# Optimization experiments

Hardware: AMD Instinct MI355X
Metric: run time of the kernel (lower is better)

## Reference

```python
import jax, jax.numpy as jnp
import numpy as np

B, C, H, W = 4, 256, 64, 64
CH = C // 2  # inner channels


def setup_inputs() -> dict:
    key = jax.random.key(0)
    ks = jax.random.split(key, 9)
    s_in = 1.0 / np.sqrt(C)
    s_w = 1.0 / np.sqrt(CH)
    return {
        "x": jax.random.normal(ks[0], (B, C, H, W), dtype=jnp.float32),
        "theta_w": jax.random.normal(ks[1], (CH, C), dtype=jnp.float32) * s_in,
        "theta_b": jax.random.normal(ks[2], (CH,), dtype=jnp.float32) * s_in,
        "phi_w": jax.random.normal(ks[3], (CH, C), dtype=jnp.float32) * s_in,
        "phi_b": jax.random.normal(ks[4], (CH,), dtype=jnp.float32) * s_in,
        "g_w": jax.random.normal(ks[5], (CH, C), dtype=jnp.float32) * s_in,
        "g_b": jax.random.normal(ks[6], (CH,), dtype=jnp.float32) * s_in,
        "W_w": jax.random.normal(ks[7], (C, CH), dtype=jnp.float32) * s_w,
        "W_b": jax.random.normal(ks[8], (C,), dtype=jnp.float32) * s_w,
    }


def _proj(x_flat, w, b):
    # 1x1 conv == channel matmul; x_flat: [B, C, N] -> [B, O, N]
    return jnp.einsum("oc,bcn->bon", w, x_flat) + b[None, :, None]


def reference(x, theta_w, theta_b, phi_w, phi_b, g_w, g_b, W_w, W_b):
    b, c, h, w = x.shape
    n = h * w
    xf = x.reshape(b, c, n)
    theta = _proj(xf, theta_w, theta_b)  # [B, CH, N]
    phi = _proj(xf, phi_w, phi_b)        # [B, CH, N]
    g = _proj(xf, g_w, g_b)              # [B, CH, N]
    # scores[b,i,j] = theta[:, :, i] . phi[:, :, j]; softmax over j
    attn = jax.nn.softmax(jnp.einsum("bci,bcj->bij", theta, phi), axis=-1)
    # torch: bmm(g_x, attn) -> out[b,c,i] = sum_j g[b,c,j] * attn[b,j,i]
    out = jnp.einsum("bcj,bji->bci", g, attn)  # [B, CH, N]
    out = jnp.einsum("oc,bcn->bon", W_w, out) + W_b[None, :, None]
    return out.reshape(b, c, h, w) + x
```

## Files before the change

### kernel.cpp

```cpp
#include <hip/hip_runtime.h>
#include <hip/hip_bf16.h>
#include <math.h>

#define BB    4
#define CC    256
#define CHN   128
#define NN    4096

typedef short short8 __attribute__((ext_vector_type(8)));
typedef float f32x4  __attribute__((ext_vector_type(4)));
typedef float f32x16 __attribute__((ext_vector_type(16)));
typedef unsigned short u16;
typedef u16  us4 __attribute__((ext_vector_type(4)));

#define MFMA16(a, b, c) __builtin_amdgcn_mfma_f32_16x16x32_bf16((a), (b), (c), 0, 0, 0)
#define MFMA32(a, b, c) __builtin_amdgcn_mfma_f32_32x32x16_bf16((a), (b), (c), 0, 0, 0)
#define LOG2E 1.4426950408889634f

#if __has_builtin(__builtin_amdgcn_exp2f)
#define EXP2F(x) __builtin_amdgcn_exp2f(x)
#else
#define EXP2F(x) exp2f(x)
#endif
#if __has_builtin(__builtin_amdgcn_logf)
#define LOG2F(x) __builtin_amdgcn_logf(x)
#else
#define LOG2F(x) log2f(x)
#endif

static __device__ __forceinline__ u16 f2bf(float f) {
    union { float f; unsigned u; } v; v.f = f;
    unsigned r = v.u + 0x7FFFu + ((v.u >> 16) & 1u);
    return (u16)(r >> 16);
}
static __device__ __forceinline__ unsigned pkbf(float a, float b) {
    __hip_bfloat162 h = __float22bfloat162_rn(make_float2(a, b));
    return *reinterpret_cast<unsigned*>(&h);
}
static __device__ __forceinline__ int sw128(int row, int u) {
    return row * 128 + ((u ^ (row & 7)) << 3);
}
static __device__ __forceinline__ void gload16(const u16* g, u16* l) {
    __builtin_amdgcn_global_load_lds(
        (const __attribute__((address_space(1))) void*)g,
        (__attribute__((address_space(3))) void*)l, 16, 0, 0);
}

typedef union { unsigned u[4]; short8 v; } bfrag;

#if __has_builtin(__builtin_amdgcn_permlane32_swap)
#define REPACK(sv, f) do { \
    unsigned e0 = pkbf(EXP2F(sv[0]),  EXP2F(sv[1])); \
    unsigned e1 = pkbf(EXP2F(sv[2]),  EXP2F(sv[3])); \
    unsigned e2 = pkbf(EXP2F(sv[4]),  EXP2F(sv[5])); \
    unsigned e3 = pkbf(EXP2F(sv[6]),  EXP2F(sv[7])); \
    unsigned e4 = pkbf(EXP2F(sv[8]),  EXP2F(sv[9])); \
    unsigned e5 = pkbf(EXP2F(sv[10]), EXP2F(sv[11])); \
    unsigned e6 = pkbf(EXP2F(sv[12]), EXP2F(sv[13])); \
    unsigned e7 = pkbf(EXP2F(sv[14]), EXP2F(sv[15])); \
    auto r02 = __builtin_amdgcn_permlane32_swap(e0, e2, false, false); \
    auto r13 = __builtin_amdgcn_permlane32_swap(e1, e3, false, false); \
    auto r46 = __builtin_amdgcn_permlane32_swap(e4, e6, false, false); \
    auto r57 = __builtin_amdgcn_permlane32_swap(e5, e7, false, false); \
    f[0].u[0] = r02[0]; f[0].u[1] = r13[0]; \
    f[0].u[2] = r02[1]; f[0].u[3] = r13[1]; \
    f[1].u[0] = r46[0]; f[1].u[1] = r57[0]; \
    f[1].u[2] = r46[1]; f[1].u[3] = r57[1]; \
} while (0)
#else
#define REPACK(sv, f) do { \
    unsigned e0 = pkbf(EXP2F(sv[0]),  EXP2F(sv[1])); \
    unsigned e1 = pkbf(EXP2F(sv[2]),  EXP2F(sv[3])); \
    unsigned e2 = pkbf(EXP2F(sv[4]),  EXP2F(sv[5])); \
    unsigned e3 = pkbf(EXP2F(sv[6]),  EXP2F(sv[7])); \
    unsigned e4 = pkbf(EXP2F(sv[8]),  EXP2F(sv[9])); \
    unsigned e5 = pkbf(EXP2F(sv[10]), EXP2F(sv[11])); \
    unsigned e6 = pkbf(EXP2F(sv[12]), EXP2F(sv[13])); \
    unsigned e7 = pkbf(EXP2F(sv[14]), EXP2F(sv[15])); \
    unsigned q0 = __shfl_xor(e0, 32), q1 = __shfl_xor(e1, 32); \
    unsigned q2 = __shfl_xor(e2, 32), q3 = __shfl_xor(e3, 32); \
    unsigned q4 = __shfl_xor(e4, 32), q5 = __shfl_xor(e5, 32); \
    unsigned q6 = __shfl_xor(e6, 32), q7 = __shfl_xor(e7, 32); \
    f[0].u[0] = lh ? q2 : e0;  f[0].u[1] = lh ? q3 : e1; \
    f[0].u[2] = lh ? e2 : q0;  f[0].u[3] = lh ? e3 : q1; \
    f[1].u[0] = lh ? q6 : e4;  f[1].u[1] = lh ? q7 : e5; \
    f[1].u[2] = lh ? e6 : q4;  f[1].u[3] = lh ? e7 : q5; \
} while (0)
#endif

__global__ __launch_bounds__(256) void k_cvtw(
    const float* __restrict__ tw, const float* __restrict__ pw,
    const float* __restrict__ gw, const float* __restrict__ Ww,
    u16* __restrict__ wall)
{
    int idx = (blockIdx.x * 256 + threadIdx.x) * 4;
    const float* s = (idx < 32768) ? tw
                   : (idx < 65536) ? pw
                   : (idx < 98304) ? gw : Ww;
    float sc = (idx < 32768) ? LOG2E : 1.0f;
    float4 v = *(const float4*)(s + (idx & 32767));
    us4 r = { f2bf(v.x * sc), f2bf(v.y * sc), f2bf(v.z * sc), f2bf(v.w * sc) };
    *(us4*)(wall + idx) = r;
}

__global__ __launch_bounds__(512) void k_proj(
    const float* __restrict__ x, const u16* __restrict__ wall,
    const float* __restrict__ tb, const float* __restrict__ pb,
    const float* __restrict__ gbias,
    u16* __restrict__ tht, u16* __restrict__ pht, u16* __restrict__ gg)
{
    __shared__ u16 xs[64 * 264];
    __shared__ u16 gbuf[128 * 68];
    const int tid = threadIdx.x;
    const int n0  = blockIdx.x * 64;
    const int b   = blockIdx.y;
    const int ln  = tid & 15, q = (tid >> 4) & 3, wid = tid >> 6;
    const int ow  = wid & 1, nw = wid >> 1;

    for (int p = 0; p < 8; ++p) {
        int id = p * 512 + tid;
        int c = id >> 4, n4 = (id & 15) * 4;
        float4 xv = *(const float4*)(x + ((size_t)b * CC + c) * NN + n0 + n4);
        xs[(n4 + 0) * 264 + c] = f2bf(xv.x);
        xs[(n4 + 1) * 264 + c] = f2bf(xv.y);
        xs[(n4 + 2) * 264 + c] = f2bf(xv.z);
        xs[(n4 + 3) * 264 + c] = f2bf(xv.w);
    }
    __syncthreads();

    short8 bfr[8];
    #pragma unroll
    for (int ks = 0; ks < 8; ++ks)
        bfr[ks] = *(const short8*)(&xs[(nw * 16 + ln) * 264 + ks * 32 + q * 8]);

    for (int pr = 0; pr < 3; ++pr) {
        const u16* wsrc = wall + pr * 32768;
        f32x4 acc[4];
        #pragma unroll
        for (int oo = 0; oo < 4; ++oo) acc[oo] = (f32x4){0.f, 0.f, 0.f, 0.f};
        for (int ks = 0; ks < 8; ++ks) {
            short8 a[4];
            #pragma unroll
            for (int oo = 0; oo < 4; ++oo)
                a[oo] = *(const short8*)(wsrc + (size_t)(ow*64 + oo*16 + ln) * 256 + ks*32 + q*8);
            #pragma unroll
            for (int oo = 0; oo < 4; ++oo)
                acc[oo] = MFMA16(a[oo], bfr[ks], acc[oo]);
        }
        const float* bias = (pr == 0) ? tb : (pr == 1 ? pb : gbias);
        const float bsc = (pr == 0) ? LOG2E : 1.0f;
        if (pr < 2) {
            u16* dst = (pr == 0) ? tht : pht;
            const int n = n0 + nw * 16 + ln;
            #pragma unroll
            for (int oo = 0; oo < 4; ++oo) {
                int o = ow * 64 + oo * 16 + q * 4;
                float4 bv = *(const float4*)(bias + o);
                f32x4 v = acc[oo];
                uint2 r = { pkbf(v.x + bv.x * bsc, v.y + bv.y * bsc),
                            pkbf(v.z + bv.z * bsc, v.w + bv.w * bsc) };
                *(uint2*)(dst + ((size_t)b * NN + n) * CHN + o) = r;
            }
        } else {
            const int nl = nw * 16 + ln;
            #pragma unroll
            for (int oo = 0; oo < 4; ++oo) {
                int o = ow * 64 + oo * 16 + q * 4;
                float4 bv = *(const float4*)(bias + o);
                f32x4 v = acc[oo];
                gbuf[(o + 0) * 68 + nl] = f2bf(v.x + bv.x);
                gbuf[(o + 1) * 68 + nl] = f2bf(v.y + bv.y);
                gbuf[(o + 2) * 68 + nl] = f2bf(v.z + bv.z);
                gbuf[(o + 3) * 68 + nl] = f2bf(v.w + bv.w);
            }
            __syncthreads();
            for (int p = 0; p < 4; ++p) {
                int id = p * 512 + tid;
                int c = id >> 4, n4 = (id & 15) * 4;
                us4 r = *(const us4*)(&gbuf[c * 68 + n4]);
                *(us4*)(gg + ((size_t)b * CHN + c) * NN + n0 + n4) = r;
            }
        }
    }
}

__global__ __launch_bounds__(512, 2) void k_rowsum(
    const u16* __restrict__ tht, const u16* __restrict__ pht,
    float* __restrict__ Z)
{
    __shared__ u16 ph_s[2][128 * 128];
    const int tid = threadIdx.x;
    const int j0  = blockIdx.x * 256;
    const int i00 = blockIdx.y * 1024;
    const int b   = blockIdx.z;
    const int l   = tid & 63, w = tid >> 6;
    const int lm  = l & 31, lh = l >> 5;
    const u16* thb = tht + (size_t)b * NN * CHN;
    const u16* phb = pht + (size_t)b * NN * CHN;

    short8 ar[8];
    #pragma unroll
    for (int ks = 0; ks < 8; ++ks)
        ar[ks] = *(const short8*)(thb + (size_t)(j0 + w*32 + lm) * CHN + ks*16 + lh*8);

    for (int p = 0; p < 4; ++p) {
        int id = p * 512 + tid;
        int row = id >> 4, u = id & 15;
        short8 v = *(const short8*)(phb + (size_t)(i00 + row) * CHN + u * 8);
        *(short8*)(&ph_s[0][sw128(row, u)]) = v;
    }

    float zp[16];
    #pragma unroll
    for (int r = 0; r < 16; ++r) zp[r] = 0.f;

    for (int is = 0; is < 8; ++is) {
        __syncthreads();
        if (is < 7) {
            for (int p = 0; p < 4; ++p) {
                int id = p * 512 + tid;
                int row = id >> 4, u = id & 15;
                short8 v = *(const short8*)(phb + (size_t)(i00 + (is+1)*128 + row) * CHN + u * 8);
                *(short8*)(&ph_s[(is + 1) & 1][sw128(row, u)]) = v;
            }
        }
        const u16* cur = ph_s[is & 1];

        #pragma unroll
        for (int ii = 0; ii < 4; ++ii) {
            f32x16 s;
            #pragma unroll
            for (int r = 0; r < 16; ++r) s[r] = 0.f;
            #pragma unroll
            for (int ks = 0; ks < 8; ++ks) {
                short8 bfrag = *(const short8*)(&cur[sw128(ii*32 + lm, ks*2 + lh)]);
                s = MFMA32(ar[ks], bfrag, s);
            }
            #pragma unroll
            for (int r = 0; r < 16; ++r) zp[r] += EXP2F(s[r]);
        }
    }

    float zr[16];
    #pragma unroll
    for (int r = 0; r < 16; ++r) {
        float v = zp[r];
        v += __shfl_xor(v, 1);
        v += __shfl_xor(v, 2);
        v += __shfl_xor(v, 4);
        v += __shfl_xor(v, 8);
        v += __shfl_xor(v, 16);
        zr[r] = v;
    }
    if (lm == 0) {
        #pragma unroll
        for (int r = 0; r < 16; ++r) {
            int j = j0 + w*32 + (r & 3) + 8*(r >> 2) + 4*lh;
            atomicAdd(&Z[(size_t)b * NN + j], zr[r]);
        }
    }
}

__global__ __launch_bounds__(256) void k_log(
    const float* __restrict__ Z, float* __restrict__ L)
{
    int idx = (blockIdx.x * 256 + threadIdx.x) * 4;
    float4 z = *(const float4*)(Z + idx);
    float4 r = { -LOG2F(z.x), -LOG2F(z.y), -LOG2F(z.z), -LOG2F(z.w) };
    *(float4*)(L + idx) = r;
}

__global__ __launch_bounds__(256, 2) void k_attn(
    const u16* __restrict__ tht, const u16* __restrict__ pht,
    const u16* __restrict__ gg, const float* __restrict__ Lbuf,
    u16* __restrict__ innerT)
{
    __shared__ u16 th_s[2][32 * 128];
    __shared__ u16 g_s [2][64 * 64];
    const int tid = threadIdx.x;
    const int i0  = blockIdx.x * 128;
    const int jq  = blockIdx.y;
    const int b   = blockIdx.z;
    const int w   = tid >> 6;
    const int lm  = tid & 31, lh = (tid >> 5) & 1;

    const u16*  thb = tht + (size_t)b * NN * CHN;
    const u16*  ggb = gg  + (size_t)b * CHN * NN;
    const float* Lb = Lbuf + (size_t)b * NN;

    int offT[2], offG[2];
    #pragma unroll
    for (int p = 0; p < 2; ++p) {
        int id = p * 256 + tid;
        int rT = id >> 4, uT = (id & 15) ^ (rT & 7);
        offT[p] = rT * CHN + uT * 8;
        int R = id >> 3, gi = (id & 7) ^ (R & 7);
        offG[p] = (((R << 1) | (gi >> 2)) * NN) + (gi & 3) * 8;
    }

    short8 phr[8];
    #pragma unroll
    for (int ks = 0; ks < 8; ++ks)
        phr[ks] = *(const short8*)(pht + ((size_t)b * NN + i0 + w*32 + lm) * CHN + ks*16 + lh*8);

    #pragma unroll
    for (int p = 0; p < 2; ++p) {
        gload16(thb + (size_t)(jq * 512) * CHN + offT[p], &th_s[0][0] + p*2048 + tid*8);
        gload16(ggb + jq * 512 + offG[p],                 &g_s [0][0] + p*2048 + tid*8);
    }
    __syncthreads();

    f32x16 pacc[4];
    #pragma unroll
    for (int ct = 0; ct < 4; ++ct)
        #pragma unroll
        for (int r = 0; r < 16; ++r) pacc[ct][r] = 0.f;

    for (int s = 0; s < 16; ++s) {
        const int j0s = jq * 512 + s * 32;
        const u16* thc = th_s[s & 1];
        const u16* gc  = g_s [s & 1];

        if (s < 15) {
            const int nb = (s + 1) & 1;
            #pragma unroll
            for (int p = 0; p < 2; ++p) {
                gload16(thb + (size_t)(j0s + 32) * CHN + offT[p], &th_s[nb][0] + p*2048 + tid*8);
                gload16(ggb + (j0s + 32) + offG[p],               &g_s [nb][0] + p*2048 + tid*8);
            }
        }

        f32x16 sv;
        #pragma unroll
        for (int rq = 0; rq < 4; ++rq) {
            float4 Lv = *(const float4*)(Lb + j0s + rq*8 + lh*4);
            sv[rq*4 + 0] = Lv.x; sv[rq*4 + 1] = Lv.y;
            sv[rq*4 + 2] = Lv.z; sv[rq*4 + 3] = Lv.w;
        }
        #pragma unroll
        for (int ks = 0; ks < 8; ++ks) {
            short8 a = *(const short8*)(&thc[sw128(lm, ks*2 + lh)]);
            sv = MFMA32(a, phr[ks], sv);
        }
        bfrag f[2];
        REPACK(sv, f);
        #pragma unroll
        for (int h = 0; h < 2; ++h) {
            #pragma unroll
            for (int ct = 0; ct < 4; ++ct) {
                const int c  = ct*32 + lm;
                const int R  = c >> 1;
                const int ch = (((c & 1) << 2) | (h*2 + lh)) ^ (R & 7);
                short8 ag = *(const short8*)(&gc[R*64 + ch*8]);
                pacc[ct] = MFMA32(ag, f[h].v, pacc[ct]);
            }
        }
        __syncthreads();
    }

    u16* dst = innerT + ((size_t)jq * BB + b) * (size_t)NN * CHN;
    const int i = i0 + w*32 + lm;
    #pragma unroll
    for (int ct = 0; ct < 4; ++ct) {
        #pragma unroll
        for (int rq = 0; rq < 4; ++rq) {
            const int c0 = ct*32 + rq*8 + lh*4;
            uint2 r = { pkbf(pacc[ct][rq*4+0], pacc[ct][rq*4+1]),
                        pkbf(pacc[ct][rq*4+2], pacc[ct][rq*4+3]) };
            *(uint2*)(dst + (size_t)i * CHN + c0) = r;
        }
    }
}

__global__ __launch_bounds__(512, 2) void k_final(
    const u16* __restrict__ innerT, const float* __restrict__ x,
    const u16* __restrict__ Wwbf, const float* __restrict__ Wb,
    float* __restrict__ out)
{
    __shared__ u16 w_s[256 * 128];
    __shared__ u16 a_s[64 * 128];
    const int tid = threadIdx.x;
    const int n0  = blockIdx.x * 64;
    const int b   = blockIdx.y;
    const int l   = tid & 63, w = tid >> 6;
    const int lm  = l & 31, lh = l >> 5;

    for (int p = 0; p < 8; ++p) {
        int id = p * 512 + tid;
        int row = id >> 4, u = id & 15;
        *(short8*)(&w_s[sw128(row, u)]) = *(const short8*)(Wwbf + (size_t)row * CHN + u * 8);
    }
    __syncthreads();

    short8 aw[8];
    #pragma unroll
    for (int ks = 0; ks < 8; ++ks)
        aw[ks] = *(const short8*)(&w_s[sw128(w*32 + lm, ks*2 + lh)]);

    f32x16 acc[2];
    #pragma unroll
    for (int nt = 0; nt < 2; ++nt)
        #pragma unroll
        for (int r = 0; r < 16; ++r) acc[nt][r] = 0.f;

    for (int jq = 0; jq < 8; ++jq) {
        __syncthreads();
        for (int p = 0; p < 2; ++p) {
            int id = p * 512 + tid;
            int row = id >> 4, u = id & 15;
            *(short8*)(&a_s[sw128(row, u)]) =
                *(const short8*)(innerT + (((size_t)jq * BB + b) * NN + n0 + row) * CHN + u * 8);
        }
        __syncthreads();
        #pragma unroll
        for (int ks = 0; ks < 8; ++ks) {
            short8 bn[2];
            #pragma unroll
            for (int nt = 0; nt < 2; ++nt)
                bn[nt] = *(const short8*)(&a_s[sw128(nt*32 + lm, ks*2 + lh)]);
            acc[0] = MFMA32(aw[ks], bn[0], acc[0]);
            acc[1] = MFMA32(aw[ks], bn[1], acc[1]);
        }
    }

    #pragma unroll
    for (int nt = 0; nt < 2; ++nt) {
        const int n = n0 + nt*32 + lm;
        #pragma unroll
        for (int r = 0; r < 16; ++r) {
            const int o = w*32 + (r & 3) + 8*(r >> 2) + 4*lh;
            const size_t idx = ((size_t)b * CC + o) * NN + n;
            out[idx] = acc[nt][r] + Wb[o] + x[idx];
        }
    }
}

extern "C" void kernel_launch(void* const* d_in, const int* in_sizes, int n_in,
                              void* d_out, int out_size, void* d_ws, size_t ws_size,
                              hipStream_t stream)
{
    const float* x  = (const float*)d_in[0];
    const float* tw = (const float*)d_in[1];
    const float* tb = (const float*)d_in[2];
    const float* pw = (const float*)d_in[3];
    const float* pb = (const float*)d_in[4];
    const float* gw = (const float*)d_in[5];
    const float* gb = (const float*)d_in[6];
    const float* Ww = (const float*)d_in[7];
    const float* Wb = (const float*)d_in[8];
    float* out = (float*)d_out;

    char* p = (char*)d_ws;
    const size_t proj_u16 = (size_t)BB * NN * CHN;
    u16*   tht    = (u16*)p;   p += proj_u16 * 2;
    u16*   pht    = (u16*)p;   p += proj_u16 * 2;
    u16*   gg     = (u16*)p;   p += proj_u16 * 2;
    u16*   wall   = (u16*)p;   p += (size_t)131072 * 2;
    float* Z      = (float*)p; p += (size_t)BB * NN * 4;
    float* Lbuf   = (float*)p; p += (size_t)BB * NN * 4;
    u16*   innerT = (u16*)p;

    hipMemsetAsync(Z, 0, (size_t)BB * NN * sizeof(float), stream);
    k_cvtw  <<<128, 256, 0, stream>>>(tw, pw, gw, Ww, wall);
    k_proj  <<<dim3(64, BB), 512, 0, stream>>>(x, wall, tb, pb, gb, tht, pht, gg);
    k_rowsum<<<dim3(16, 4, BB), 512, 0, stream>>>(tht, pht, Z);
    k_log   <<<16, 256, 0, stream>>>(Z, Lbuf);
    k_attn  <<<dim3(32, 8, BB), 256, 0, stream>>>(tht, pht, gg, Lbuf, innerT);
    k_final <<<dim3(64, BB), 512, 0, stream>>>(innerT, x, wall + 98304, Wb, out);
}
```

Baseline: 207.9 us.

## Drop LDS staging in rowsum/attn, load operands from global, halve j-split

```diff
diff --git a/kernel.cpp b/kernel.cpp
--- a/kernel.cpp
+++ b/kernel.cpp
@@ -39,11 +39,6 @@
 }
 static __device__ __forceinline__ int sw128(int row, int u) {
     return row * 128 + ((u ^ (row & 7)) << 3);
-}
-static __device__ __forceinline__ void gload16(const u16* g, u16* l) {
-    __builtin_amdgcn_global_load_lds(
-        (const __attribute__((address_space(1))) void*)g,
-        (__attribute__((address_space(3))) void*)l, 16, 0, 0);
 }
 
 typedef union { unsigned u[4]; short8 v; } bfrag;
@@ -188,7 +183,6 @@
     const u16* __restrict__ tht, const u16* __restrict__ pht,
     float* __restrict__ Z)
 {
-    __shared__ u16 ph_s[2][128 * 128];
     const int tid = threadIdx.x;
     const int j0  = blockIdx.x * 256;
     const int i00 = blockIdx.y * 1024;
@@ -203,42 +197,26 @@
     for (int ks = 0; ks < 8; ++ks)
         ar[ks] = *(const short8*)(thb + (size_t)(j0 + w*32 + lm) * CHN + ks*16 + lh*8);
 
-    for (int p = 0; p < 4; ++p) {
-        int id = p * 512 + tid;
-        int row = id >> 4, u = id & 15;
-        short8 v = *(const short8*)(phb + (size_t)(i00 + row) * CHN + u * 8);
-        *(short8*)(&ph_s[0][sw128(row, u)]) = v;
-    }
-
     float zp[16];
     #pragma unroll
     for (int r = 0; r < 16; ++r) zp[r] = 0.f;
 
-    for (int is = 0; is < 8; ++is) {
-        __syncthreads();
-        if (is < 7) {
-            for (int p = 0; p < 4; ++p) {
-                int id = p * 512 + tid;
-                int row = id >> 4, u = id & 15;
-                short8 v = *(const short8*)(phb + (size_t)(i00 + (is+1)*128 + row) * CHN + u * 8);
-                *(short8*)(&ph_s[(is + 1) & 1][sw128(row, u)]) = v;
-            }
-        }
-        const u16* cur = ph_s[is & 1];
-
-        #pragma unroll
-        for (int ii = 0; ii < 4; ++ii) {
-            f32x16 s;
-            #pragma unroll
-            for (int r = 0; r < 16; ++r) s[r] = 0.f;
-            #pragma unroll
-            for (int ks = 0; ks < 8; ++ks) {
-                short8 bfrag = *(const short8*)(&cur[sw128(ii*32 + lm, ks*2 + lh)]);
-                s = MFMA32(ar[ks], bfrag, s);
-            }
-            #pragma unroll
-            for (int r = 0; r < 16; ++r) zp[r] += EXP2F(s[r]);
-        }
+    const u16* prow = phb + (size_t)(i00 + lm) * CHN + lh*8;
+    for (int ii = 0; ii < 32; ++ii) {
+        short8 bf[8];
+        #pragma unroll
+        for (int ks = 0; ks < 8; ++ks)
+            bf[ks] = *(const short8*)(prow + (size_t)ii * 32 * CHN + ks*16);
+        f32x16 s;
+        #pragma unroll
+        for (int r = 0; r < 16; ++r) s[r] = 0.f;
+        __builtin_amdgcn_s_setprio(1);
+        #pragma unroll
+        for (int ks = 0; ks < 8; ++ks)
+            s = MFMA32(ar[ks], bf[ks], s);
+        __builtin_amdgcn_s_setprio(0);
+        #pragma unroll
+        for (int r = 0; r < 16; ++r) zp[r] += EXP2F(s[r]);
     }
 
     float zr[16];
@@ -270,13 +248,11 @@
     *(float4*)(L + idx) = r;
 }
 
-__global__ __launch_bounds__(256, 2) void k_attn(
+__global__ __launch_bounds__(256) void k_attn(
     const u16* __restrict__ tht, const u16* __restrict__ pht,
     const u16* __restrict__ gg, const float* __restrict__ Lbuf,
     u16* __restrict__ innerT)
 {
-    __shared__ u16 th_s[2][32 * 128];
-    __shared__ u16 g_s [2][64 * 64];
     const int tid = threadIdx.x;
     const int i0  = blockIdx.x * 128;
     const int jq  = blockIdx.y;
@@ -288,48 +264,26 @@
     const u16*  ggb = gg  + (size_t)b * CHN * NN;
     const float* Lb = Lbuf + (size_t)b * NN;
 
-    int offT[2], offG[2];
-    #pragma unroll
-    for (int p = 0; p < 2; ++p) {
-        int id = p * 256 + tid;
-        int rT = id >> 4, uT = (id & 15) ^ (rT & 7);
-        offT[p] = rT * CHN + uT * 8;
-        int R = id >> 3, gi = (id & 7) ^ (R & 7);
-        offG[p] = (((R << 1) | (gi >> 2)) * NN) + (gi & 3) * 8;
-    }
-
     short8 phr[8];
     #pragma unroll
     for (int ks = 0; ks < 8; ++ks)
         phr[ks] = *(const short8*)(pht + ((size_t)b * NN + i0 + w*32 + lm) * CHN + ks*16 + lh*8);
 
-    #pragma unroll
-    for (int p = 0; p < 2; ++p) {
-        gload16(thb + (size_t)(jq * 512) * CHN + offT[p], &th_s[0][0] + p*2048 + tid*8);
-        gload16(ggb + jq * 512 + offG[p],                 &g_s [0][0] + p*2048 + tid*8);
-    }
-    __syncthreads();
-
     f32x16 pacc[4];
     #pragma unroll
     for (int ct = 0; ct < 4; ++ct)
         #pragma unroll
         for (int r = 0; r < 16; ++r) pacc[ct][r] = 0.f;
 
-    for (int s = 0; s < 16; ++s) {
-        const int j0s = jq * 512 + s * 32;
-        const u16* thc = th_s[s & 1];
-        const u16* gc  = g_s [s & 1];
-
-        if (s < 15) {
-            const int nb = (s + 1) & 1;
-            #pragma unroll
-            for (int p = 0; p < 2; ++p) {
-                gload16(thb + (size_t)(j0s + 32) * CHN + offT[p], &th_s[nb][0] + p*2048 + tid*8);
-                gload16(ggb + (j0s + 32) + offG[p],               &g_s [nb][0] + p*2048 + tid*8);
-            }
-        }
-
+    const u16* throw_ = thb + (size_t)(jq*1024 + lm) * CHN + lh*8;
+    const u16* grow   = ggb + (size_t)lm * NN + jq*1024 + lh*8;
+
+    for (int jj = 0; jj < 32; ++jj) {
+        const int j0s = jq*1024 + jj*32;
+        short8 a[8];
+        #pragma unroll
+        for (int ks = 0; ks < 8; ++ks)
+            a[ks] = *(const short8*)(throw_ + (size_t)jj * 32 * CHN + ks*16);
         f32x16 sv;
         #pragma unroll
         for (int rq = 0; rq < 4; ++rq) {
@@ -337,25 +291,23 @@
             sv[rq*4 + 0] = Lv.x; sv[rq*4 + 1] = Lv.y;
             sv[rq*4 + 2] = Lv.z; sv[rq*4 + 3] = Lv.w;
         }
-        #pragma unroll
-        for (int ks = 0; ks < 8; ++ks) {
-            short8 a = *(const short8*)(&thc[sw128(lm, ks*2 + lh)]);
-            sv = MFMA32(a, phr[ks], sv);
-        }
+        __builtin_amdgcn_s_setprio(1);
+        #pragma unroll
+        for (int ks = 0; ks < 8; ++ks)
+            sv = MFMA32(a[ks], phr[ks], sv);
+        __builtin_amdgcn_s_setprio(0);
         bfrag f[2];
         REPACK(sv, f);
+        __builtin_amdgcn_s_setprio(1);
         #pragma unroll
         for (int h = 0; h < 2; ++h) {
             #pragma unroll
             for (int ct = 0; ct < 4; ++ct) {
-                const int c  = ct*32 + lm;
-                const int R  = c >> 1;
-                const int ch = (((c & 1) << 2) | (h*2 + lh)) ^ (R & 7);
-                short8 ag = *(const short8*)(&gc[R*64 + ch*8]);
+                short8 ag = *(const short8*)(grow + (size_t)ct * 32 * NN + jj*32 + h*16);
                 pacc[ct] = MFMA32(ag, f[h].v, pacc[ct]);
             }
         }
-        __syncthreads();
+        __builtin_amdgcn_s_setprio(0);
     }
 
     u16* dst = innerT + ((size_t)jq * BB + b) * (size_t)NN * CHN;
@@ -403,7 +355,7 @@
         #pragma unroll
         for (int r = 0; r < 16; ++r) acc[nt][r] = 0.f;
 
-    for (int jq = 0; jq < 8; ++jq) {
+    for (int jq = 0; jq < 4; ++jq) {
         __syncthreads();
         for (int p = 0; p < 2; ++p) {
             int id = p * 512 + tid;
@@ -465,6 +417,6 @@
     k_proj  <<<dim3(64, BB), 512, 0, stream>>>(x, wall, tb, pb, gb, tht, pht, gg);
     k_rowsum<<<dim3(16, 4, BB), 512, 0, stream>>>(tht, pht, Z);
     k_log   <<<16, 256, 0, stream>>>(Z, Lbuf);
-    k_attn  <<<dim3(32, 8, BB), 256, 0, stream>>>(tht, pht, gg, Lbuf, innerT);
+    k_attn  <<<dim3(32, 4, BB), 256, 0, stream>>>(tht, pht, gg, Lbuf, innerT);
     k_final <<<dim3(64, BB), 512, 0, stream>>>(innerT, x, wall + 98304, Wb, out);
 }
```

Result: slower. 325.9 us (+56.8%).
